# Kernel tuning notes

Hardware: AMD Instinct MI355X
Metric: run time of the kernel (lower is better)

## Reference

```python
import jax, jax.numpy as jnp
import numpy as np
from jax import lax

N_GAUSS = 4096


def setup_inputs() -> dict:
    key = jax.random.key(0)
    k1, k2, k3, k4 = jax.random.split(key, 4)
    return {
        "_xyz": jax.random.normal(k1, (N_GAUSS, 3), dtype=jnp.float32),
        "_scaling": jax.random.normal(k2, (N_GAUSS, 3), dtype=jnp.float32),
        "_rotation": jax.random.normal(k3, (N_GAUSS, 4), dtype=jnp.float32),
        "_opacity": jax.random.normal(k4, (N_GAUSS, 1), dtype=jnp.float32),
        "resolution": 64,
        "num_blocks": 16,
    }


def _extract_fields(_xyz, _scaling, _rotation, _opacity, resolution, num_blocks):
    relax_ratio = 1.5
    block_size = 2.0 / num_blocks
    split_size = resolution // num_blocks

    # opacity activation + threshold mask (kept dense; masked gaussians get 0 weight)
    opacities = jax.nn.sigmoid(_opacity)[:, 0]  # [N]
    keep = opacities > 0.005
    opa = jnp.where(keep, opacities, 0.0)

    BIG = jnp.float32(1e10)
    mn = jnp.min(jnp.where(keep[:, None], _xyz, BIG), axis=0)
    mx = jnp.max(jnp.where(keep[:, None], _xyz, -BIG), axis=0)
    center = (mn + mx) / 2
    scale = 1.8 / jnp.max(mx - mn)
    xyzs = (_xyz - center) * scale           # [N,3] normalized positions
    stds = jnp.exp(_scaling) * scale         # [N,3] scaling activation * scale

    # covariance from scaling+rotation: L = R @ diag(s); C = L L^T
    q = _rotation / jnp.linalg.norm(_rotation, axis=1, keepdims=True)
    r, x, y, z = q[:, 0], q[:, 1], q[:, 2], q[:, 3]
    R = jnp.stack([
        jnp.stack([1 - 2 * (y * y + z * z), 2 * (x * y - r * z), 2 * (x * z + r * y)], -1),
        jnp.stack([2 * (x * y + r * z), 1 - 2 * (x * x + z * z), 2 * (y * z - r * x)], -1),
        jnp.stack([2 * (x * z - r * y), 2 * (y * z + r * x), 1 - 2 * (x * x + y * y)], -1),
    ], axis=1)                               # [N,3,3]
    L = R * stds[:, None, :]                 # R @ diag(s)
    C = jnp.einsum('nij,nkj->nik', L, L)     # [N,3,3]
    a, b, c = C[:, 0, 0], C[:, 0, 1], C[:, 0, 2]
    d, e, f = C[:, 1, 1], C[:, 1, 2], C[:, 2, 2]

    # analytic 3x3 symmetric inverse (precomputed per gaussian)
    inv_det = 1.0 / (a * d * f + 2 * e * c * b - e * e * a - c * c * d - b * b * f + 1e-24)
    inv_a = (d * f - e * e) * inv_det
    inv_b = (e * c - b * f) * inv_det
    inv_c = (e * b - c * d) * inv_det
    inv_d = (a * f - c * c) * inv_det
    inv_e = (b * c - e * a) * inv_det
    inv_f = (a * d - b * b) * inv_det

    lin = jnp.linspace(-1.0, 1.0, resolution).astype(jnp.float32)
    nb = num_blocks
    bi, bj, bk = jnp.meshgrid(jnp.arange(nb), jnp.arange(nb), jnp.arange(nb), indexing='ij')
    blocks = jnp.stack([bi.ravel(), bj.ravel(), bk.ravel()], axis=1)  # [nb^3, 3]
    off = jnp.arange(split_size)
    relax = block_size * relax_ratio

    def block_val(blk):
        xs = lin[blk[0] * split_size + off]
        ys = lin[blk[1] * split_size + off]
        zs = lin[blk[2] * split_size + off]
        xx, yy, zz = jnp.meshgrid(xs, ys, zs, indexing='ij')
        pts = jnp.stack([xx.ravel(), yy.ravel(), zz.ravel()], axis=-1)  # [S^3, 3]
        vmin = pts.min(0) - relax
        vmax = pts.max(0) + relax
        inside = jnp.all((xyzs < vmax) & (xyzs > vmin), axis=1)  # [N]
        w_opa = jnp.where(inside, opa, 0.0)                      # [N]
        dxyz = pts[:, None, :] - xyzs[None, :, :]                # [S^3, N, 3]
        px, py, pz = dxyz[..., 0], dxyz[..., 1], dxyz[..., 2]
        power = (-0.5 * (px * px * inv_a + py * py * inv_d + pz * pz * inv_f)
                 - px * py * inv_b - px * pz * inv_c - py * pz * inv_e)
        power = jnp.where(power > 0, jnp.float32(-1e10), power)
        val = jnp.sum(w_opa * jnp.exp(power), axis=1)            # [S^3]
        return val.reshape(split_size, split_size, split_size)

    vals = lax.map(block_val, blocks)  # [nb^3, S, S, S]
    occ = (vals.reshape(nb, nb, nb, split_size, split_size, split_size)
               .transpose(0, 3, 1, 4, 2, 5)
               .reshape(resolution, resolution, resolution))
    return occ


def reference(_xyz, _scaling, _rotation, _opacity, resolution, num_blocks):
    return _extract_fields(_xyz, _scaling, _rotation, _opacity, resolution, num_blocks)
```

## Files before the change

kernel.cpp:

```cpp
#include <hip/hip_runtime.h>

#define NG 4096
#define RELAX 0.1875f
#define KEEPTH -5.2933049f

__device__ __forceinline__ float linf(int i) { return -1.0f + (2.0f/63.0f)*(float)i; }
__device__ __forceinline__ int cperm(int i) { return (i & 1) ? 7 + ((i+1)>>1) : 7 - (i>>1); }

template<int T>
__device__ __forceinline__ float4 block_minmax_cs(
    const float4* __restrict__ xyz4, const float4* __restrict__ op4,
    int tid, float (*s_r)[6])
{
  float mn0=1e10f, mn1=1e10f, mn2=1e10f;
  float mx0=-1e10f, mx1=-1e10f, mx2=-1e10f;
  #pragma unroll
  for (int t = 0; t < NG/4/T; ++t) {
    const int G = t*T + tid;
    float4 v0 = xyz4[3*G+0], v1 = xyz4[3*G+1], v2 = xyz4[3*G+2];
    float4 oo = op4[G];
    if (oo.x > KEEPTH) { mn0=fminf(mn0,v0.x); mx0=fmaxf(mx0,v0.x);
                         mn1=fminf(mn1,v0.y); mx1=fmaxf(mx1,v0.y);
                         mn2=fminf(mn2,v0.z); mx2=fmaxf(mx2,v0.z); }
    if (oo.y > KEEPTH) { mn0=fminf(mn0,v0.w); mx0=fmaxf(mx0,v0.w);
                         mn1=fminf(mn1,v1.x); mx1=fmaxf(mx1,v1.x);
                         mn2=fminf(mn2,v1.y); mx2=fmaxf(mx2,v1.y); }
    if (oo.z > KEEPTH) { mn0=fminf(mn0,v1.z); mx0=fmaxf(mx0,v1.z);
                         mn1=fminf(mn1,v1.w); mx1=fmaxf(mx1,v1.w);
                         mn2=fminf(mn2,v2.x); mx2=fmaxf(mx2,v2.x); }
    if (oo.w > KEEPTH) { mn0=fminf(mn0,v2.y); mx0=fmaxf(mx0,v2.y);
                         mn1=fminf(mn1,v2.z); mx1=fmaxf(mx1,v2.z);
                         mn2=fminf(mn2,v2.w); mx2=fmaxf(mx2,v2.w); }
  }
  #pragma unroll
  for (int s = 1; s < 64; s <<= 1) {
    mn0 = fminf(mn0, __shfl_xor(mn0, s)); mx0 = fmaxf(mx0, __shfl_xor(mx0, s));
    mn1 = fminf(mn1, __shfl_xor(mn1, s)); mx1 = fmaxf(mx1, __shfl_xor(mx1, s));
    mn2 = fminf(mn2, __shfl_xor(mn2, s)); mx2 = fmaxf(mx2, __shfl_xor(mx2, s));
  }
  if ((tid & 63) == 0) {
    const int w = tid >> 6;
    s_r[w][0]=mn0; s_r[w][1]=mn1; s_r[w][2]=mn2;
    s_r[w][3]=mx0; s_r[w][4]=mx1; s_r[w][5]=mx2;
  }
  __syncthreads();
  mn0 = s_r[0][0]; mn1 = s_r[0][1]; mn2 = s_r[0][2];
  mx0 = s_r[0][3]; mx1 = s_r[0][4]; mx2 = s_r[0][5];
  #pragma unroll
  for (int w = 1; w < T/64; ++w) {
    mn0 = fminf(mn0, s_r[w][0]); mn1 = fminf(mn1, s_r[w][1]); mn2 = fminf(mn2, s_r[w][2]);
    mx0 = fmaxf(mx0, s_r[w][3]); mx1 = fmaxf(mx1, s_r[w][4]); mx2 = fmaxf(mx2, s_r[w][5]);
  }
  return make_float4((mn0+mx0)*0.5f, (mn1+mx1)*0.5f, (mn2+mx2)*0.5f,
                     1.8f/fmaxf(mx0-mn0, fmaxf(mx1-mn1, mx2-mn2)));
}

__device__ __forceinline__ void transform_one(
    const float* __restrict__ xyz, const float* __restrict__ scal,
    const float* __restrict__ rot, const float* __restrict__ opac,
    int g, float cx, float cy, float cz, float sc,
    float4* __restrict__ pos, float4* __restrict__ inv)
{
  float o = opac[g];
  float sig = 1.0f/(1.0f + __expf(-o));
  float opa = (sig > 0.005f) ? sig : 0.0f;
  float xs = (xyz[3*g+0]-cx)*sc;
  float ys = (xyz[3*g+1]-cy)*sc;
  float zs = (xyz[3*g+2]-cz)*sc;
  float sdx = __expf(scal[3*g+0])*sc;
  float sdy = __expf(scal[3*g+1])*sc;
  float sdz = __expf(scal[3*g+2])*sc;
  float qr=rot[4*g+0], qx=rot[4*g+1], qy=rot[4*g+2], qz=rot[4*g+3];
  float qn = 1.0f/sqrtf(qr*qr+qx*qx+qy*qy+qz*qz);
  qr*=qn; qx*=qn; qy*=qn; qz*=qn;
  float R00 = 1.0f-2.0f*(qy*qy+qz*qz), R01 = 2.0f*(qx*qy-qr*qz), R02 = 2.0f*(qx*qz+qr*qy);
  float R10 = 2.0f*(qx*qy+qr*qz), R11 = 1.0f-2.0f*(qx*qx+qz*qz), R12 = 2.0f*(qy*qz-qr*qx);
  float R20 = 2.0f*(qx*qz-qr*qy), R21 = 2.0f*(qy*qz+qr*qx), R22 = 1.0f-2.0f*(qx*qx+qy*qy);
  float L00=R00*sdx, L01=R01*sdy, L02=R02*sdz;
  float L10=R10*sdx, L11=R11*sdy, L12=R12*sdz;
  float L20=R20*sdx, L21=R21*sdy, L22=R22*sdz;
  float a = L00*L00+L01*L01+L02*L02;
  float bb= L00*L10+L01*L11+L02*L12;
  float cc= L00*L20+L01*L21+L02*L22;
  float d = L10*L10+L11*L11+L12*L12;
  float e = L10*L20+L11*L21+L12*L22;
  float f = L20*L20+L21*L21+L22*L22;
  float det = a*d*f + 2.0f*e*cc*bb - e*e*a - cc*cc*d - bb*bb*f + 1e-24f;
  float idt = 1.0f/det;
  float ia=(d*f-e*e)*idt, ib=(e*cc-bb*f)*idt, ic=(e*bb-cc*d)*idt;
  float id=(a*f-cc*cc)*idt, ie=(bb*cc-e*a)*idt, iff=(a*d-bb*bb)*idt;
  pos[g]     = make_float4(xs, ys, zs, opa);
  inv[2*g+0] = make_float4(-0.5f*ia, -ib, -ic, -0.5f*id);
  inv[2*g+1] = make_float4(-ie, -0.5f*iff, 0.0f, 0.0f);
}

__global__ __launch_bounds__(512) void gm_prep(
    const float* __restrict__ xyz, const float* __restrict__ scal,
    const float* __restrict__ rot, const float* __restrict__ opac,
    float4* __restrict__ pos, float4* __restrict__ inv)
{
  __shared__ float s_r[8][6];
  const int tid = threadIdx.x;
  const int b   = blockIdx.x;
  const float4* xyz4 = (const float4*)xyz;
  const float4* op4  = (const float4*)opac;
  const float4 cs = block_minmax_cs<512>(xyz4, op4, tid, s_r);
  if (tid < 16)
    transform_one(xyz, scal, rot, opac, b*16+tid, cs.x, cs.y, cs.z, cs.w, pos, inv);
}

__global__ __launch_bounds__(512) void gm_eval(
    const float4* __restrict__ pos, const float4* __restrict__ inv,
    float* __restrict__ out)
{
  __shared__ float4 s_g[8][64*3];
  __shared__ float  s_p[8][64];
  const int tid  = threadIdx.x;
  const int w    = tid >> 6;
  const int lane = tid & 63;
  const int b = blockIdx.x;
  const int bi = cperm(b >> 8), bj = cperm((b >> 4) & 15), bk = cperm(b & 15);
  const float vminx = linf(bi*4) - RELAX, vmaxx = linf(bi*4+3) + RELAX;
  const float vminy = linf(bj*4) - RELAX, vmaxy = linf(bj*4+3) + RELAX;
  const float vminz = linf(bk*4) - RELAX, vmaxz = linf(bk*4+3) + RELAX;
  const int sx = lane >> 4, sy = (lane >> 2) & 3, sz = lane & 3;
  const float ptx = linf(bi*4+sx), pty = linf(bj*4+sy), ptz = linf(bk*4+sz);
  const int gbase = w*512 + lane;
  float acc = 0.0f;

  float4 P = pos[gbase];
  #pragma unroll
  for (int scn = 0; scn < 8; ++scn) {
    const int g = gbase + scn*64;
    float4 Pn;
    if (scn < 7) Pn = pos[g + 64];
    const bool pass = (P.w > 0.0f &&
                       P.x > vminx && P.x < vmaxx &&
                       P.y > vminy && P.y < vmaxy &&
                       P.z > vminz && P.z < vmaxz);
    const unsigned long long mask = __ballot(pass);
    const int m = __popcll(mask);
    if (m != 0) {
      if (pass) {
        const int slot = __popcll(mask & ((1ull << lane) - 1ull));
        s_g[w][3*slot+0] = P;
        s_g[w][3*slot+1] = inv[2*g+0];
        s_g[w][3*slot+2] = inv[2*g+1];
      }
      __builtin_amdgcn_wave_barrier();
      for (int j = 0; j < m; ++j) {
        float4 Pq = s_g[w][3*j+0];
        float4 I0 = s_g[w][3*j+1];
        float4 I1 = s_g[w][3*j+2];
        float px = ptx - Pq.x, py = pty - Pq.y, pz = ptz - Pq.z;
        float power = px*px*I0.x + py*py*I0.w + pz*pz*I1.y
                    + px*py*I0.y + px*pz*I0.z + py*pz*I1.x;
        power = (power > 0.0f) ? -1e10f : power;
        acc += Pq.w * __expf(power);
      }
      __builtin_amdgcn_wave_barrier();
    }
    P = Pn;
  }

  s_p[w][lane] = acc;
  __syncthreads();
  if (w == 0) {
    float v = 0.0f;
    #pragma unroll
    for (int q = 0; q < 8; ++q) v += s_p[q][lane];
    out[(bi*4+sx)*4096 + (bj*4+sy)*64 + (bk*4+sz)] = v;
  }
}

__global__ __launch_bounds__(256) void gm_fused_nows(
    const float* __restrict__ xyz, const float* __restrict__ scal,
    const float* __restrict__ rot, const float* __restrict__ opac,
    float* __restrict__ out)
{
  __shared__ float s_r[8][6];
  __shared__ float4 s_g[256*3];
  __shared__ float  s_acc[256];
  __shared__ int    s_cnt;
  const int tid = threadIdx.x;
  const float4* xyz4 = (const float4*)xyz;
  const float4* op4  = (const float4*)opac;
  if (tid == 0) s_cnt = 0;
  const float4 cs = block_minmax_cs<256>(xyz4, op4, tid, s_r);
  const float cx = cs.x, cy = cs.y, cz = cs.z, sc = cs.w;

  const int bin = blockIdx.x;
  const int bi = bin >> 8, bj = (bin >> 4) & 15, bk = bin & 15;
  const float vminx = linf(bi*4) - RELAX, vmaxx = linf(bi*4+3) + RELAX;
  const float vminy = linf(bj*4) - RELAX, vmaxy = linf(bj*4+3) + RELAX;
  const float vminz = linf(bk*4) - RELAX, vmaxz = linf(bk*4+3) + RELAX;
  const int p    = tid & 63;
  const int part = tid >> 6;
  const int sx = p >> 4, sy = (p >> 2) & 3, sz = p & 3;
  const float ptx = linf(bi*4+sx), pty = linf(bj*4+sy), ptz = linf(bk*4+sz);
  float acc = 0.0f;
  __syncthreads();

  for (int c0 = 0; c0 < NG; c0 += 256) {
    const int g = c0 + tid;
    float o = opac[g];
    bool pass = false;
    float xs=0, ys=0, zs=0, sig=0;
    if (o > KEEPTH) {
      sig = 1.0f/(1.0f + __expf(-o));
      xs = (xyz[3*g+0]-cx)*sc;
      ys = (xyz[3*g+1]-cy)*sc;
      zs = (xyz[3*g+2]-cz)*sc;
      pass = xs > vminx && xs < vmaxx &&
             ys > vminy && ys < vmaxy &&
             zs > vminz && zs < vmaxz;
    }
    if (pass) {
      float sdx = __expf(scal[3*g+0])*sc;
      float sdy = __expf(scal[3*g+1])*sc;
      float sdz = __expf(scal[3*g+2])*sc;
      float qr=rot[4*g+0], qx=rot[4*g+1], qy=rot[4*g+2], qz=rot[4*g+3];
      float qn = 1.0f/sqrtf(qr*qr+qx*qx+qy*qy+qz*qz);
      qr*=qn; qx*=qn; qy*=qn; qz*=qn;
      float R00 = 1.0f-2.0f*(qy*qy+qz*qz), R01 = 2.0f*(qx*qy-qr*qz), R02 = 2.0f*(qx*qz+qr*qy);
      float R10 = 2.0f*(qx*qy+qr*qz), R11 = 1.0f-2.0f*(qx*qx+qz*qz), R12 = 2.0f*(qy*qz-qr*qx);
      float R20 = 2.0f*(qx*qz-qr*qy), R21 = 2.0f*(qy*qz+qr*qx), R22 = 1.0f-2.0f*(qx*qx+qy*qy);
      float L00=R00*sdx, L01=R01*sdy, L02=R02*sdz;
      float L10=R10*sdx, L11=R11*sdy, L12=R12*sdz;
      float L20=R20*sdx, L21=R21*sdy, L22=R22*sdz;
      float a = L00*L00+L01*L01+L02*L02;
      float bb= L00*L10+L01*L11+L02*L12;
      float cc= L00*L20+L01*L21+L02*L22;
      float d = L10*L10+L11*L11+L12*L12;
      float e = L10*L20+L11*L21+L12*L22;
      float f = L20*L20+L21*L21+L22*L22;
      float det = a*d*f + 2.0f*e*cc*bb - e*e*a - cc*cc*d - bb*bb*f + 1e-24f;
      float idt = 1.0f/det;
      float ia=(d*f-e*e)*idt, ib=(e*cc-bb*f)*idt, ic=(e*bb-cc*d)*idt;
      float id=(a*f-cc*cc)*idt, ie=(bb*cc-e*a)*idt, iff=(a*d-bb*bb)*idt;
      int slot = atomicAdd(&s_cnt, 1);
      s_g[3*slot+0] = make_float4(xs, ys, zs, sig);
      s_g[3*slot+1] = make_float4(-0.5f*ia, -ib, -ic, -0.5f*id);
      s_g[3*slot+2] = make_float4(-ie, -0.5f*iff, 0.0f, 0.0f);
    }
    __syncthreads();
    const int nn = s_cnt;
    #pragma unroll 4
    for (int j = part; j < nn; j += 4) {
      float4 P  = s_g[3*j+0];
      float4 I0 = s_g[3*j+1];
      float4 I1 = s_g[3*j+2];
      float px = ptx - P.x, py = pty - P.y, pz = ptz - P.z;
      float power = px*px*I0.x + py*py*I0.w + pz*pz*I1.y
                  + px*py*I0.y + px*pz*I0.z + py*pz*I1.x;
      power = (power > 0.0f) ? -1e10f : power;
      acc += P.w * __expf(power);
    }
    __syncthreads();
    if (tid == 0) s_cnt = 0;
    __syncthreads();
  }
  s_acc[tid] = acc;
  __syncthreads();
  if (tid < 64) {
    float v = s_acc[tid] + s_acc[tid+64] + s_acc[tid+128] + s_acc[tid+192];
    out[(bi*4+sx)*4096 + (bj*4+sy)*64 + (bk*4+sz)] = v;
  }
}

extern "C" void kernel_launch(void* const* d_in, const int* in_sizes, int n_in,
                              void* d_out, int out_size, void* d_ws, size_t ws_size,
                              hipStream_t stream) {
  const float* xyz  = (const float*)d_in[0];
  const float* scal = (const float*)d_in[1];
  const float* rot  = (const float*)d_in[2];
  const float* opac = (const float*)d_in[3];
  float* out = (float*)d_out;
  char* ws = (char*)d_ws;
  float4* pos = (float4*)ws;
  float4* inv = (float4*)(ws + 65536);

  if (ws_size >= 196608) {
    gm_prep<<<256, 512, 0, stream>>>(xyz, scal, rot, opac, pos, inv);
    gm_eval<<<4096, 512, 0, stream>>>(pos, inv, out);
  } else {
    gm_fused_nows<<<4096, 256, 0, stream>>>(xyz, scal, rot, opac, out);
  }
}
```

Measured before the change: 112.0 us.

## Evaluate four spatial blocks per workgroup sharing one gaussian scan

gm_eval now handles four voxel blocks per workgroup. Each block is chosen by a strided rank permutation that mixes center and edge blocks for load balance. Each gaussian is loaded and culled once against all four block bounds, compacted with a per-block flag mask, and evaluated only for the blocks it overlaps. The grid shrinks from 4096 to 1024 workgroups, which amortizes the position/inverse loads and the ballot/compaction overhead. In exchange it adds divergent per-flag branches, more registers, and fewer workgroups to fill the GPU.

```diff
diff --git a/kernel.cpp b/kernel.cpp
--- a/kernel.cpp
+++ b/kernel.cpp
@@ -114,61 +114,105 @@
     float* __restrict__ out)
 {
   __shared__ float4 s_g[8][64*3];
-  __shared__ float  s_p[8][64];
+  __shared__ int    s_f[8][64];
+  __shared__ float  s_p[8][4][64];
   const int tid  = threadIdx.x;
   const int w    = tid >> 6;
   const int lane = tid & 63;
   const int b = blockIdx.x;
-  const int bi = cperm(b >> 8), bj = cperm((b >> 4) & 15), bk = cperm(b & 15);
-  const float vminx = linf(bi*4) - RELAX, vmaxx = linf(bi*4+3) + RELAX;
-  const float vminy = linf(bj*4) - RELAX, vmaxy = linf(bj*4+3) + RELAX;
-  const float vminz = linf(bk*4) - RELAX, vmaxz = linf(bk*4+3) + RELAX;
   const int sx = lane >> 4, sy = (lane >> 2) & 3, sz = lane & 3;
-  const float ptx = linf(bi*4+sx), pty = linf(bj*4+sy), ptz = linf(bk*4+sz);
+
+  float vmnx[4], vmxx[4], vmny[4], vmxy[4], vmnz[4], vmxz[4];
+  float ptx[4], pty[4], ptz[4];
+  #pragma unroll
+  for (int q = 0; q < 4; ++q) {
+    const int rank = q*1024 + ((b + q*331) & 1023);
+    const int bi = cperm(rank >> 8), bj = cperm((rank >> 4) & 15), bk = cperm(rank & 15);
+    vmnx[q] = linf(bi*4) - RELAX; vmxx[q] = linf(bi*4+3) + RELAX;
+    vmny[q] = linf(bj*4) - RELAX; vmxy[q] = linf(bj*4+3) + RELAX;
+    vmnz[q] = linf(bk*4) - RELAX; vmxz[q] = linf(bk*4+3) + RELAX;
+    ptx[q] = linf(bi*4+sx); pty[q] = linf(bj*4+sy); ptz[q] = linf(bk*4+sz);
+  }
+
+  float acc0 = 0.0f, acc1 = 0.0f, acc2 = 0.0f, acc3 = 0.0f;
   const int gbase = w*512 + lane;
-  float acc = 0.0f;
-
   float4 P = pos[gbase];
-  #pragma unroll
-  for (int scn = 0; scn < 8; ++scn) {
-    const int g = gbase + scn*64;
+
+  #pragma unroll
+  for (int t = 0; t < 8; ++t) {
+    const int g = gbase + t*64;
     float4 Pn;
-    if (scn < 7) Pn = pos[g + 64];
-    const bool pass = (P.w > 0.0f &&
-                       P.x > vminx && P.x < vmaxx &&
-                       P.y > vminy && P.y < vmaxy &&
-                       P.z > vminz && P.z < vmaxz);
-    const unsigned long long mask = __ballot(pass);
-    const int m = __popcll(mask);
-    if (m != 0) {
-      if (pass) {
+    if (t < 7) Pn = pos[g + 64];
+    int flags = 0;
+    if (P.w > 0.0f) {
+      #pragma unroll
+      for (int q = 0; q < 4; ++q) {
+        if (P.x > vmnx[q] && P.x < vmxx[q] &&
+            P.y > vmny[q] && P.y < vmxy[q] &&
+            P.z > vmnz[q] && P.z < vmxz[q]) flags |= (1 << q);
+      }
+    }
+    const unsigned long long mask = __ballot(flags != 0);
+    const int mU = __popcll(mask);
+    if (mU != 0) {
+      if (flags) {
         const int slot = __popcll(mask & ((1ull << lane) - 1ull));
         s_g[w][3*slot+0] = P;
         s_g[w][3*slot+1] = inv[2*g+0];
         s_g[w][3*slot+2] = inv[2*g+1];
+        s_f[w][slot] = flags;
       }
       __builtin_amdgcn_wave_barrier();
-      for (int j = 0; j < m; ++j) {
-        float4 Pq = s_g[w][3*j+0];
-        float4 I0 = s_g[w][3*j+1];
-        float4 I1 = s_g[w][3*j+2];
-        float px = ptx - Pq.x, py = pty - Pq.y, pz = ptz - Pq.z;
-        float power = px*px*I0.x + py*py*I0.w + pz*pz*I1.y
-                    + px*py*I0.y + px*pz*I0.z + py*pz*I1.x;
-        power = (power > 0.0f) ? -1e10f : power;
-        acc += Pq.w * __expf(power);
+      for (int s = 0; s < mU; ++s) {
+        const float4 Pq = s_g[w][3*s+0];
+        const float4 I0 = s_g[w][3*s+1];
+        const float4 I1 = s_g[w][3*s+2];
+        const int fl = s_f[w][s];
+        if (fl & 1) {
+          float px = ptx[0]-Pq.x, py = pty[0]-Pq.y, pz = ptz[0]-Pq.z;
+          float power = px*px*I0.x + py*py*I0.w + pz*pz*I1.y
+                      + px*py*I0.y + px*pz*I0.z + py*pz*I1.x;
+          power = (power > 0.0f) ? -1e10f : power;
+          acc0 += Pq.w * __expf(power);
+        }
+        if (fl & 2) {
+          float px = ptx[1]-Pq.x, py = pty[1]-Pq.y, pz = ptz[1]-Pq.z;
+          float power = px*px*I0.x + py*py*I0.w + pz*pz*I1.y
+                      + px*py*I0.y + px*pz*I0.z + py*pz*I1.x;
+          power = (power > 0.0f) ? -1e10f : power;
+          acc1 += Pq.w * __expf(power);
+        }
+        if (fl & 4) {
+          float px = ptx[2]-Pq.x, py = pty[2]-Pq.y, pz = ptz[2]-Pq.z;
+          float power = px*px*I0.x + py*py*I0.w + pz*pz*I1.y
+                      + px*py*I0.y + px*pz*I0.z + py*pz*I1.x;
+          power = (power > 0.0f) ? -1e10f : power;
+          acc2 += Pq.w * __expf(power);
+        }
+        if (fl & 8) {
+          float px = ptx[3]-Pq.x, py = pty[3]-Pq.y, pz = ptz[3]-Pq.z;
+          float power = px*px*I0.x + py*py*I0.w + pz*pz*I1.y
+                      + px*py*I0.y + px*pz*I0.z + py*pz*I1.x;
+          power = (power > 0.0f) ? -1e10f : power;
+          acc3 += Pq.w * __expf(power);
+        }
       }
       __builtin_amdgcn_wave_barrier();
     }
     P = Pn;
   }
 
-  s_p[w][lane] = acc;
+  s_p[w][0][lane] = acc0;
+  s_p[w][1][lane] = acc1;
+  s_p[w][2][lane] = acc2;
+  s_p[w][3][lane] = acc3;
   __syncthreads();
-  if (w == 0) {
+  if (w < 4) {
+    const int rank = w*1024 + ((b + w*331) & 1023);
+    const int bi = cperm(rank >> 8), bj = cperm((rank >> 4) & 15), bk = cperm(rank & 15);
     float v = 0.0f;
     #pragma unroll
-    for (int q = 0; q < 8; ++q) v += s_p[q][lane];
+    for (int u = 0; u < 8; ++u) v += s_p[u][w][lane];
     out[(bi*4+sx)*4096 + (bj*4+sy)*64 + (bk*4+sz)] = v;
   }
 }
@@ -282,7 +326,7 @@
 
   if (ws_size >= 196608) {
     gm_prep<<<256, 512, 0, stream>>>(xyz, scal, rot, opac, pos, inv);
-    gm_eval<<<4096, 512, 0, stream>>>(pos, inv, out);
+    gm_eval<<<1024, 512, 0, stream>>>(pos, inv, out);
   } else {
     gm_fused_nows<<<4096, 256, 0, stream>>>(xyz, scal, rot, opac, out);
   }
```

Result: no change. 113.5 us (+1.4%).

## Split gaussian range across eight blocks per voxel tile with atomic accumulation

Applied to the files above, without the earlier changes.

The eval kernel now launches eight 256-thread blocks per 4x4x4 voxel tile, each covering a 512-gaussian slice. Each block compacts the passing gaussians block-wide through a shared atomic counter, exits early if none pass, and has four thread groups share the compacted list. Partial sums go to the output with global float atomics, so the output is zeroed with a memset first. The aim is finer-grained parallelism and better load balance across tiles, at the cost of an extra memset, more blocks, atomic traffic, and a summation order that is no longer deterministic.

```diff
diff --git a/kernel.cpp b/kernel.cpp
--- a/kernel.cpp
+++ b/kernel.cpp
@@ -109,67 +109,63 @@
     transform_one(xyz, scal, rot, opac, b*16+tid, cs.x, cs.y, cs.z, cs.w, pos, inv);
 }
 
-__global__ __launch_bounds__(512) void gm_eval(
+__global__ __launch_bounds__(256) void gm_eval(
     const float4* __restrict__ pos, const float4* __restrict__ inv,
     float* __restrict__ out)
 {
-  __shared__ float4 s_g[8][64*3];
-  __shared__ float  s_p[8][64];
+  __shared__ float4 s_g[512*3];
+  __shared__ float  s_acc[256];
+  __shared__ int    s_cnt;
   const int tid  = threadIdx.x;
-  const int w    = tid >> 6;
-  const int lane = tid & 63;
-  const int b = blockIdx.x;
-  const int bi = cperm(b >> 8), bj = cperm((b >> 4) & 15), bk = cperm(b & 15);
+  const int blk  = blockIdx.x;
+  const int rank = blk >> 3;
+  const int sl   = blk & 7;
+  const int bi = cperm(rank >> 8), bj = cperm((rank >> 4) & 15), bk = cperm(rank & 15);
   const float vminx = linf(bi*4) - RELAX, vmaxx = linf(bi*4+3) + RELAX;
   const float vminy = linf(bj*4) - RELAX, vmaxy = linf(bj*4+3) + RELAX;
   const float vminz = linf(bk*4) - RELAX, vmaxz = linf(bk*4+3) + RELAX;
-  const int sx = lane >> 4, sy = (lane >> 2) & 3, sz = lane & 3;
+  if (tid == 0) s_cnt = 0;
+  __syncthreads();
+
+  #pragma unroll
+  for (int t = 0; t < 2; ++t) {
+    const int g = sl*512 + t*256 + tid;
+    float4 P = pos[g];
+    if (P.w > 0.0f &&
+        P.x > vminx && P.x < vmaxx &&
+        P.y > vminy && P.y < vmaxy &&
+        P.z > vminz && P.z < vmaxz) {
+      int slot = atomicAdd(&s_cnt, 1);
+      s_g[3*slot+0] = P;
+      s_g[3*slot+1] = inv[2*g+0];
+      s_g[3*slot+2] = inv[2*g+1];
+    }
+  }
+  __syncthreads();
+  const int n = s_cnt;
+  if (n == 0) return;
+
+  const int p    = tid & 63;
+  const int part = tid >> 6;
+  const int sx = p >> 4, sy = (p >> 2) & 3, sz = p & 3;
   const float ptx = linf(bi*4+sx), pty = linf(bj*4+sy), ptz = linf(bk*4+sz);
-  const int gbase = w*512 + lane;
   float acc = 0.0f;
-
-  float4 P = pos[gbase];
-  #pragma unroll
-  for (int scn = 0; scn < 8; ++scn) {
-    const int g = gbase + scn*64;
-    float4 Pn;
-    if (scn < 7) Pn = pos[g + 64];
-    const bool pass = (P.w > 0.0f &&
-                       P.x > vminx && P.x < vmaxx &&
-                       P.y > vminy && P.y < vmaxy &&
-                       P.z > vminz && P.z < vmaxz);
-    const unsigned long long mask = __ballot(pass);
-    const int m = __popcll(mask);
-    if (m != 0) {
-      if (pass) {
-        const int slot = __popcll(mask & ((1ull << lane) - 1ull));
-        s_g[w][3*slot+0] = P;
-        s_g[w][3*slot+1] = inv[2*g+0];
-        s_g[w][3*slot+2] = inv[2*g+1];
-      }
-      __builtin_amdgcn_wave_barrier();
-      for (int j = 0; j < m; ++j) {
-        float4 Pq = s_g[w][3*j+0];
-        float4 I0 = s_g[w][3*j+1];
-        float4 I1 = s_g[w][3*j+2];
-        float px = ptx - Pq.x, py = pty - Pq.y, pz = ptz - Pq.z;
-        float power = px*px*I0.x + py*py*I0.w + pz*pz*I1.y
-                    + px*py*I0.y + px*pz*I0.z + py*pz*I1.x;
-        power = (power > 0.0f) ? -1e10f : power;
-        acc += Pq.w * __expf(power);
-      }
-      __builtin_amdgcn_wave_barrier();
-    }
-    P = Pn;
-  }
-
-  s_p[w][lane] = acc;
-  __syncthreads();
-  if (w == 0) {
-    float v = 0.0f;
-    #pragma unroll
-    for (int q = 0; q < 8; ++q) v += s_p[q][lane];
-    out[(bi*4+sx)*4096 + (bj*4+sy)*64 + (bk*4+sz)] = v;
+  #pragma unroll 4
+  for (int j = part; j < n; j += 4) {
+    float4 P  = s_g[3*j+0];
+    float4 I0 = s_g[3*j+1];
+    float4 I1 = s_g[3*j+2];
+    float px = ptx - P.x, py = pty - P.y, pz = ptz - P.z;
+    float power = px*px*I0.x + py*py*I0.w + pz*pz*I1.y
+                + px*py*I0.y + px*pz*I0.z + py*pz*I1.x;
+    power = (power > 0.0f) ? -1e10f : power;
+    acc += P.w * __expf(power);
+  }
+  s_acc[tid] = acc;
+  __syncthreads();
+  if (tid < 64) {
+    float v = s_acc[tid] + s_acc[tid+64] + s_acc[tid+128] + s_acc[tid+192];
+    atomicAdd(&out[(bi*4+sx)*4096 + (bj*4+sy)*64 + (bk*4+sz)], v);
   }
 }
 
@@ -281,8 +277,9 @@
   float4* inv = (float4*)(ws + 65536);
 
   if (ws_size >= 196608) {
+    hipMemsetAsync(out, 0, out_size, stream);
     gm_prep<<<256, 512, 0, stream>>>(xyz, scal, rot, opac, pos, inv);
-    gm_eval<<<4096, 512, 0, stream>>>(pos, inv, out);
+    gm_eval<<<4096*8, 256, 0, stream>>>(pos, inv, out);
   } else {
     gm_fused_nows<<<4096, 256, 0, stream>>>(xyz, scal, rot, opac, out);
   }
```

Result: faster. 103.8 us (-7.3%).
